# Kernel tuning notes

Measured on AMD Instinct MI355X. Metric: run time of the kernel, lower is better.

The kernel has to match this reference:

```python
import jax, jax.numpy as jnp
import numpy as np

B, T, P, H, D = 8, 16, 14, 16, 64
L = P * P            # 196 patches (CLS excluded)
DM = H * D           # 1024 = d_model
NS = 16              # n_synos
T2 = T * T           # 256 = n_frames**2


def _conv2d(x, w, b):
    # x: [N,C,H,W], w: [O,I,kh,kw], stride 1, SAME padding (ksize//2 for odd k)
    y = jax.lax.conv_general_dilated(x, w, (1, 1), 'SAME',
                                     dimension_numbers=('NCHW', 'OIHW', 'NCHW'))
    return y + b[None, :, None, None]


def _layernorm(x, g, b):
    m = x.mean(-1, keepdims=True)
    v = x.var(-1, keepdims=True)
    return (x - m) / jnp.sqrt(v + 1e-5) * g + b


def setup_inputs() -> dict:
    key = jax.random.key(0)
    ks = jax.random.split(key, 12)
    q = jax.random.normal(ks[0], (B, T, L + 1, H, D), jnp.float32)
    k = jax.random.normal(ks[1], (B, T, L + 1, H, D), jnp.float32)
    v = jax.random.normal(ks[2], (B, T, L + 1, H, D), jnp.float32)
    syno_emb = jax.random.normal(ks[3], (NS, DM), jnp.float32) * 0.02
    t_conv_w = jax.random.normal(ks[4], (1, 2 * H, 3, 3), jnp.float32) * 0.001
    t_conv_b = jnp.zeros((1,), jnp.float32)
    ln_g = jnp.ones((T2,), jnp.float32)
    ln_b = jnp.zeros((T2,), jnp.float32)
    w1 = jax.random.normal(ks[5], (T2, T2), jnp.float32) * 0.02
    b1 = jnp.zeros((T2,), jnp.float32)
    w2 = jax.random.normal(ks[6], (T2, T2), jnp.float32) * 0.02
    b2 = jnp.zeros((T2,), jnp.float32)
    p_conv_w = jax.random.normal(ks[7], (1, T2, 3, 3), jnp.float32) * 0.001
    p_conv_b = jnp.zeros((1,), jnp.float32)
    return dict(q=q, k=k, v=v, syno_emb=syno_emb,
                t_conv_w=t_conv_w, t_conv_b=t_conv_b,
                ln_g=ln_g, ln_b=ln_b, w1=w1, b1=b1, w2=w2, b2=b2,
                p_conv_w=p_conv_w, p_conv_b=p_conv_b)


def reference(q, k, v, syno_emb, t_conv_w, t_conv_b, ln_g, ln_b,
              w1, b1, w2, b2, p_conv_w, p_conv_b):
    # ---------------- temporal detection ----------------
    def head_aff(a):  # a: [B,T,L,H,D] -> [B*L, H, T, T]
        a = a.transpose(0, 2, 1, 3, 4)  # [B,L,T,H,D]
        scale = 1.0 / (a.shape[-1] ** 0.5)
        aff = jnp.einsum('nlqhc,nlkhc->nlqkh', a * scale, a)  # [B,L,T,T,H]
        aff = jax.nn.softmax(aff, axis=-2)  # softmax over key frames
        return aff.reshape(B * L, T, T, H).transpose(0, 3, 1, 2)

    affs = jnp.concatenate([head_aff(q[:, :, 1:]), head_aff(k[:, :, 1:])],
                           axis=1)                      # [B*L, 2H, T, T]
    aff = _conv2d(affs, t_conv_w, t_conv_b)             # [B*L, 1, T, T]
    aff = aff.reshape(B, P, P, T2)                      # [B, P, P, T^2]
    h = _layernorm(aff, ln_g, ln_b)
    h = h @ w1.T + b1
    h = jax.nn.gelu(h, approximate=False)               # torch nn.GELU default
    h = h @ w2.T + b2
    aff = aff + h
    aff = aff.transpose(0, 3, 1, 2)                     # [B, T^2, P, P]
    aff = _conv2d(aff, p_conv_w, p_conv_b)              # [B, 1, P, P]
    y_t = aff.reshape(B, -1)                            # [B, P*P]

    # ---------------- spatial detection ----------------
    kf = k[:, :, 1:].reshape(B, T, L, DM)
    vf = v[:, :, 1:].reshape(B, T, L, DM)
    s_scale = 1.0 / (DM ** 0.5)
    s_aff = jnp.einsum('qw,ntkw->ntqk', syno_emb * s_scale, kf)  # [B,T,NS,L]
    s_aff = jax.nn.softmax(s_aff, axis=-1)
    s_mix = jnp.einsum('ntql,ntlw->ntqw', s_aff, vf)    # [B,T,NS,DM]
    y_s = s_mix.reshape(B, T * NS, DM).mean(axis=1)     # [B, DM]

    return (y_t, y_s)
```

## Files before the change

kernel.cpp:

```cpp
#include <hip/hip_runtime.h>
#include <hip/hip_bf16.h>
#include <math.h>

#define BB 8
#define TT 16
#define PP 14
#define LL 196
#define HH 16
#define DD 64
#define DM 1024
#define NS 16
#define T2 256
#define LP1 197

using bf16x8 = __attribute__((ext_vector_type(8))) short;
using f32x4  = __attribute__((ext_vector_type(4))) float;

__device__ __forceinline__ float dot4(float4 a, float4 b) {
    return a.x*b.x + a.y*b.y + a.z*b.z + a.w*b.w;
}

__device__ __forceinline__ uint32_t pkbf(float lo, float hi) {
    uint32_t a = __builtin_bit_cast(uint32_t, lo);
    uint32_t b = __builtin_bit_cast(uint32_t, hi);
    a += 0x7FFFu + ((a >> 16) & 1u);
    b += 0x7FFFu + ((b >> 16) & 1u);
    return (a >> 16) | (b & 0xFFFF0000u);
}

__device__ __forceinline__ void split2(float x, float y, uint32_t* h, uint32_t* lo) {
    const uint32_t hh = pkbf(x, y);
    const float hx = __builtin_bit_cast(float, hh << 16);
    const float hy = __builtin_bit_cast(float, hh & 0xFFFF0000u);
    *h = hh;
    *lo = pkbf(x - hx, y - hy);
}

__device__ __forceinline__ void pksplit(float4 p, float4 q, bf16x8& hi, bf16x8& lo) {
    uint32_t uh[4], ul[4];
    split2(p.x, p.y, &uh[0], &ul[0]);
    split2(p.z, p.w, &uh[1], &ul[1]);
    split2(q.x, q.y, &uh[2], &ul[2]);
    split2(q.z, q.w, &uh[3], &ul[3]);
    struct U4 { uint32_t v[4]; } th, tl;
    th.v[0] = uh[0]; th.v[1] = uh[1]; th.v[2] = uh[2]; th.v[3] = uh[3];
    tl.v[0] = ul[0]; tl.v[1] = ul[1]; tl.v[2] = ul[2]; tl.v[3] = ul[3];
    hi = __builtin_bit_cast(bf16x8, th);
    lo = __builtin_bit_cast(bf16x8, tl);
}

__global__ __launch_bounds__(256) void kprep(
        const float* __restrict__ syno,
        uint32_t* __restrict__ synoHi, uint32_t* __restrict__ synoLo) {
    const int i = blockIdx.x * 256 + threadIdx.x;
    const float x = syno[2 * i], y = syno[2 * i + 1];
    uint32_t h, lo;
    split2(x, y, &h, &lo);
    synoHi[i] = h;
    synoLo[i] = lo;
}

__global__ __launch_bounds__(256) void k1_temporal(
        const float* __restrict__ qin, const float* __restrict__ kin,
        const float* __restrict__ tw,  const float* __restrict__ tbv,
        const uint32_t* __restrict__ synoHi, const uint32_t* __restrict__ synoLo,
        float* __restrict__ affRaw, float* __restrict__ SLout) {
    __shared__ __align__(16) float lds_c[256 * 36];
    __shared__ __align__(16) float lds_wf[9 * 32];
    __shared__ __align__(16) float sl_part[4][16][16];

    const int bid = blockIdx.x, b = bid / LL, l = bid % LL;
    const int tid = threadIdx.x, wid = tid >> 6, lane = tid & 63;
    const int mrow = lane & 15;
    const int g = lane >> 4;

    for (int i = tid; i < 288; i += 256) {
        const int kk = i >> 5, ch = i & 31;
        lds_wf[kk * 32 + ch] = tw[ch * 9 + kk];
    }

    const size_t rowbase = ((size_t)(b*TT + mrow)*LP1 + 1 + l)*DM + g*8;
    f32x4 acc_sl = {0.f, 0.f, 0.f, 0.f};

    #pragma unroll
    for (int j = 0; j < 4; ++j) {
        #pragma unroll
        for (int hf = 0; hf < 2; ++hf) {
            const int ch = 2*wid + 8*j + hf;
            const float* sp2 = (ch < 16) ? qin : kin;
            const float* base = sp2 + rowbase + (size_t)(ch & 15)*DD;
            const float4 a0 = *reinterpret_cast<const float4*>(base);
            const float4 a1 = *reinterpret_cast<const float4*>(base + 4);
            const float4 a2 = *reinterpret_cast<const float4*>(base + 32);
            const float4 a3 = *reinterpret_cast<const float4*>(base + 36);
            bf16x8 h1, l1, h2, l2;
            pksplit(a0, a1, h1, l1);
            pksplit(a2, a3, h2, l2);
            f32x4 acc = {0.f, 0.f, 0.f, 0.f};
            acc = __builtin_amdgcn_mfma_f32_16x16x32_bf16(h1, h1, acc, 0, 0, 0);
            acc = __builtin_amdgcn_mfma_f32_16x16x32_bf16(h1, l1, acc, 0, 0, 0);
            acc = __builtin_amdgcn_mfma_f32_16x16x32_bf16(l1, h1, acc, 0, 0, 0);
            acc = __builtin_amdgcn_mfma_f32_16x16x32_bf16(h2, h2, acc, 0, 0, 0);
            acc = __builtin_amdgcn_mfma_f32_16x16x32_bf16(h2, l2, acc, 0, 0, 0);
            acc = __builtin_amdgcn_mfma_f32_16x16x32_bf16(l2, h2, acc, 0, 0, 0);
            if (ch >= 16) {
                const int off = (lane & 15) * 512 + (ch - 16) * 32 + g * 4;
                const bf16x8 sh1 = *reinterpret_cast<const bf16x8*>(synoHi + off);
                const bf16x8 sl1 = *reinterpret_cast<const bf16x8*>(synoLo + off);
                const bf16x8 sh2 = *reinterpret_cast<const bf16x8*>(synoHi + off + 16);
                const bf16x8 sl2 = *reinterpret_cast<const bf16x8*>(synoLo + off + 16);
                acc_sl = __builtin_amdgcn_mfma_f32_16x16x32_bf16(h1, sh1, acc_sl, 0, 0, 0);
                acc_sl = __builtin_amdgcn_mfma_f32_16x16x32_bf16(h1, sl1, acc_sl, 0, 0, 0);
                acc_sl = __builtin_amdgcn_mfma_f32_16x16x32_bf16(l1, sh1, acc_sl, 0, 0, 0);
                acc_sl = __builtin_amdgcn_mfma_f32_16x16x32_bf16(h2, sh2, acc_sl, 0, 0, 0);
                acc_sl = __builtin_amdgcn_mfma_f32_16x16x32_bf16(h2, sl2, acc_sl, 0, 0, 0);
                acc_sl = __builtin_amdgcn_mfma_f32_16x16x32_bf16(l2, sh2, acc_sl, 0, 0, 0);
            }
            const float x0 = acc[0]*0.125f, x1 = acc[1]*0.125f;
            const float x2 = acc[2]*0.125f, x3 = acc[3]*0.125f;
            float m0 = x0, m1 = x1, m2 = x2, m3 = x3;
            #pragma unroll
            for (int msk = 1; msk < 16; msk <<= 1) {
                m0 = fmaxf(m0, __shfl_xor(m0, msk, 64));
                m1 = fmaxf(m1, __shfl_xor(m1, msk, 64));
                m2 = fmaxf(m2, __shfl_xor(m2, msk, 64));
                m3 = fmaxf(m3, __shfl_xor(m3, msk, 64));
            }
            const float e0 = __expf(x0 - m0), e1 = __expf(x1 - m1);
            const float e2 = __expf(x2 - m2), e3 = __expf(x3 - m3);
            float s0 = e0, s1 = e1, s2 = e2, s3 = e3;
            #pragma unroll
            for (int msk = 1; msk < 16; msk <<= 1) {
                s0 += __shfl_xor(s0, msk, 64);
                s1 += __shfl_xor(s1, msk, 64);
                s2 += __shfl_xor(s2, msk, 64);
                s3 += __shfl_xor(s3, msk, 64);
            }
            const int colb = lane & 15;
            lds_c[((g*4 + 0)*16 + colb)*36 + ch] = e0 / s0;
            lds_c[((g*4 + 1)*16 + colb)*36 + ch] = e1 / s1;
            lds_c[((g*4 + 2)*16 + colb)*36 + ch] = e2 / s2;
            lds_c[((g*4 + 3)*16 + colb)*36 + ch] = e3 / s3;
        }
    }
    #pragma unroll
    for (int r = 0; r < 4; ++r)
        sl_part[wid][g * 4 + r][lane & 15] = acc_sl[r];
    __syncthreads();

    const int oq = tid >> 4, ok = tid & 15;
    float accv = tbv[0];
    #pragma unroll
    for (int ky = 0; ky < 3; ++ky) {
        const int iq = oq + ky - 1;
        if (iq < 0 || iq > 15) continue;
        #pragma unroll
        for (int kx = 0; kx < 3; ++kx) {
            const int ik = ok + kx - 1;
            if (ik < 0 || ik > 15) continue;
            const float4* dp = reinterpret_cast<const float4*>(lds_c + (iq*16 + ik)*36);
            const float4* wp = reinterpret_cast<const float4*>(lds_wf + (ky*3 + kx)*32);
            #pragma unroll
            for (int c4 = 0; c4 < 8; ++c4) accv += dot4(dp[c4], wp[c4]);
        }
    }
    affRaw[(size_t)bid * T2 + tid] = accv;

    {
        const int t = tid >> 4, qq = tid & 15;
        const float s = sl_part[0][t][qq] + sl_part[1][t][qq] +
                        sl_part[2][t][qq] + sl_part[3][t][qq];
        SLout[((size_t)(b * TT + t) * NS + qq) * LL + l] = s * 0.03125f;
    }
}

__global__ __launch_bounds__(256) void k2_mlp(
        const float* __restrict__ affRaw,
        const float* __restrict__ lng, const float* __restrict__ lnb,
        const float* __restrict__ w1, const float* __restrict__ b1,
        const float* __restrict__ w2, const float* __restrict__ b2,
        float* __restrict__ affRes) {
    __shared__ __align__(16) float lx[4 * 256];
    __shared__ __align__(16) float lln[4 * 256];
    __shared__ __align__(16) float lg[4 * 256];
    const int tid = threadIdx.x;
    const int wave = tid >> 6, lane = tid & 63;
    const int i0 = blockIdx.x * 4;
    {
        const float* xr = affRaw + (size_t)(i0 + wave) * 256;
        float4 x = reinterpret_cast<const float4*>(xr)[lane];
        float sm = x.x + x.y + x.z + x.w;
        float ss = x.x * x.x + x.y * x.y + x.z * x.z + x.w * x.w;
        #pragma unroll
        for (int m = 1; m < 64; m <<= 1) {
            sm += __shfl_xor(sm, m, 64);
            ss += __shfl_xor(ss, m, 64);
        }
        const float mean = sm * (1.f / 256.f);
        const float var = ss * (1.f / 256.f) - mean * mean;
        const float inv = rsqrtf(var + 1e-5f);
        const float4 g4 = reinterpret_cast<const float4*>(lng)[lane];
        const float4 bb = reinterpret_cast<const float4*>(lnb)[lane];
        float4 ln;
        ln.x = (x.x - mean) * inv * g4.x + bb.x;
        ln.y = (x.y - mean) * inv * g4.y + bb.y;
        ln.z = (x.z - mean) * inv * g4.z + bb.z;
        ln.w = (x.w - mean) * inv * g4.w + bb.w;
        reinterpret_cast<float4*>(lx + wave * 256)[lane] = x;
        reinterpret_cast<float4*>(lln + wave * 256)[lane] = ln;
    }
    __syncthreads();
    const int j = tid;
    float a0 = 0.f, a1 = 0.f, a2 = 0.f, a3 = 0.f;
    {
        const float4* wr = reinterpret_cast<const float4*>(w1 + (size_t)j * 256);
        const float4* l0 = reinterpret_cast<const float4*>(lln);
        const float4* l1 = reinterpret_cast<const float4*>(lln + 256);
        const float4* l2 = reinterpret_cast<const float4*>(lln + 512);
        const float4* l3 = reinterpret_cast<const float4*>(lln + 768);
        #pragma unroll 8
        for (int m4 = 0; m4 < 64; ++m4) {
            const float4 w = wr[m4];
            a0 += dot4(w, l0[m4]); a1 += dot4(w, l1[m4]);
            a2 += dot4(w, l2[m4]); a3 += dot4(w, l3[m4]);
        }
    }
    const float bj = b1[j];
    const float kInvSqrt2 = 0.70710678118654752f;
    float h0 = a0 + bj, h1 = a1 + bj, h2 = a2 + bj, h3 = a3 + bj;
    lg[0 * 256 + j] = 0.5f * h0 * (1.f + erff(h0 * kInvSqrt2));
    lg[1 * 256 + j] = 0.5f * h1 * (1.f + erff(h1 * kInvSqrt2));
    lg[2 * 256 + j] = 0.5f * h2 * (1.f + erff(h2 * kInvSqrt2));
    lg[3 * 256 + j] = 0.5f * h3 * (1.f + erff(h3 * kInvSqrt2));
    __syncthreads();
    a0 = a1 = a2 = a3 = 0.f;
    {
        const float4* wr = reinterpret_cast<const float4*>(w2 + (size_t)j * 256);
        const float4* l0 = reinterpret_cast<const float4*>(lg);
        const float4* l1 = reinterpret_cast<const float4*>(lg + 256);
        const float4* l2 = reinterpret_cast<const float4*>(lg + 512);
        const float4* l3 = reinterpret_cast<const float4*>(lg + 768);
        #pragma unroll 8
        for (int m4 = 0; m4 < 64; ++m4) {
            const float4 w = wr[m4];
            a0 += dot4(w, l0[m4]); a1 += dot4(w, l1[m4]);
            a2 += dot4(w, l2[m4]); a3 += dot4(w, l3[m4]);
        }
    }
    const float b2j = b2[j];
    affRes[(size_t)(i0 + 0) * 256 + j] = lx[0 * 256 + j] + a0 + b2j;
    affRes[(size_t)(i0 + 1) * 256 + j] = lx[1 * 256 + j] + a1 + b2j;
    affRes[(size_t)(i0 + 2) * 256 + j] = lx[2 * 256 + j] + a2 + b2j;
    affRes[(size_t)(i0 + 3) * 256 + j] = lx[3 * 256 + j] + a3 + b2j;
}

__global__ __launch_bounds__(256) void k3a_pconv(
        const float* __restrict__ affRes, const float* __restrict__ pw,
        float* __restrict__ part) {
    __shared__ __align__(16) float lpw[576];
    const int b = blockIdx.x >> 2, cc = blockIdx.x & 3;
    const int tid = threadIdx.x;
    for (int idx = tid; idx < 576; idx += 256) {
        const int kk = idx / 64, c = idx & 63;
        lpw[kk * 64 + c] = pw[(size_t)(cc * 64 + c) * 9 + kk];
    }
    __syncthreads();
    if (tid < 196) {
        const int p1 = tid / 14, p2 = tid % 14;
        float s = 0.f;
        #pragma unroll
        for (int ky = 0; ky < 3; ++ky) {
            const int ip1 = p1 + ky - 1;
            if (ip1 < 0 || ip1 > 13) continue;
            #pragma unroll
            for (int kx = 0; kx < 3; ++kx) {
                const int ip2 = p2 + kx - 1;
                if (ip2 < 0 || ip2 > 13) continue;
                const float4* ar = reinterpret_cast<const float4*>(
                    affRes + (size_t)(b * LL + ip1 * 14 + ip2) * 256 + cc * 64);
                const float4* wr = reinterpret_cast<const float4*>(lpw + (ky * 3 + kx) * 64);
                #pragma unroll
                for (int c4 = 0; c4 < 16; ++c4) s += dot4(ar[c4], wr[c4]);
            }
        }
        part[(cc * 8 + b) * 196 + tid] = s;
    }
}

__global__ void k3b_yt(const float* __restrict__ part,
                       const float* __restrict__ pcb, float* __restrict__ out) {
    const int b = blockIdx.x, tid = threadIdx.x;
    if (tid < 196) {
        float s = pcb[0];
        #pragma unroll
        for (int cc = 0; cc < 4; ++cc) s += part[(cc * 8 + b) * 196 + tid];
        out[b * 196 + tid] = s;
    }
}

__global__ __launch_bounds__(256) void k4b_softmax(
        const float* __restrict__ SL, float* __restrict__ WSUM) {
    __shared__ float lp[16 * 200];
    const int t = blockIdx.x, b = blockIdx.y;
    const int tid = threadIdx.x;
    const int qq = tid >> 4, j = tid & 15;
    const float* row = SL + (size_t)((b * TT + t) * NS + qq) * LL;
    float v[13];
    float m = -1e30f;
    #pragma unroll
    for (int i = 0; i < 13; ++i) {
        const int l = j + i * 16;
        v[i] = (l < LL) ? row[l] : -1e30f;
        m = fmaxf(m, v[i]);
    }
    #pragma unroll
    for (int msk = 1; msk < 16; msk <<= 1) m = fmaxf(m, __shfl_xor(m, msk, 64));
    float s = 0.f;
    #pragma unroll
    for (int i = 0; i < 13; ++i) {
        const int l = j + i * 16;
        v[i] = (l < LL) ? __expf(v[i] - m) : 0.f;
        s += v[i];
    }
    #pragma unroll
    for (int msk = 1; msk < 16; msk <<= 1) s += __shfl_xor(s, msk, 64);
    const float inv = 1.f / s;
    #pragma unroll
    for (int i = 0; i < 13; ++i) {
        const int l = j + i * 16;
        if (l < LL) lp[qq * 200 + l] = v[i] * inv;
    }
    __syncthreads();
    if (tid < LL) {
        float w = 0.f;
        #pragma unroll
        for (int qi = 0; qi < 16; ++qi) w += lp[qi * 200 + tid];
        WSUM[(size_t)(b * TT + t) * LL + tid] = w;
    }
}

__global__ __launch_bounds__(256) void k4c_vsum(
        const float* __restrict__ vin, const float* __restrict__ WSUM,
        float* __restrict__ PS) {
    __shared__ float lw[98];
    const int t = blockIdx.x, b = blockIdx.y, z = blockIdx.z;
    const int tid = threadIdx.x;
    const int bt = b * TT + t;
    if (tid < 98) lw[tid] = WSUM[(size_t)bt * LL + z * 98 + tid];
    __syncthreads();
    float4 acc = make_float4(0.f, 0.f, 0.f, 0.f);
    const float* vb = vin + ((size_t)bt * LP1 + 1 + z * 98) * DM + tid * 4;
    #pragma unroll 4
    for (int l = 0; l < 98; ++l) {
        const float4 v = *reinterpret_cast<const float4*>(vb + (size_t)l * DM);
        const float w = lw[l];
        acc.x += w * v.x; acc.y += w * v.y; acc.z += w * v.z; acc.w += w * v.w;
    }
    *reinterpret_cast<float4*>(PS + ((size_t)bt * 2 + z) * DM + tid * 4) = acc;
}

__global__ void k4d_ys(const float* __restrict__ PS, float* __restrict__ out) {
    const int i = blockIdx.x * 256 + threadIdx.x;
    const int b = i >> 10, w = i & 1023;
    float s = 0.f;
    #pragma unroll
    for (int tz = 0; tz < 32; ++tz) s += PS[((size_t)b * 32 + tz) * DM + w];
    out[1568 + i] = s * (1.f / 256.f);
}

extern "C" void kernel_launch(void* const* d_in, const int* in_sizes, int n_in,
                              void* d_out, int out_size, void* d_ws, size_t ws_size,
                              hipStream_t stream) {
    const float* q    = (const float*)d_in[0];
    const float* k    = (const float*)d_in[1];
    const float* v    = (const float*)d_in[2];
    const float* syno = (const float*)d_in[3];
    const float* tw   = (const float*)d_in[4];
    const float* tbv  = (const float*)d_in[5];
    const float* lng  = (const float*)d_in[6];
    const float* lnb  = (const float*)d_in[7];
    const float* w1   = (const float*)d_in[8];
    const float* b1   = (const float*)d_in[9];
    const float* w2   = (const float*)d_in[10];
    const float* b2   = (const float*)d_in[11];
    const float* pw   = (const float*)d_in[12];
    const float* pcb  = (const float*)d_in[13];
    float* out = (float*)d_out;

    float* ws = (float*)d_ws;
    float* affRaw = ws;
    float* affRes = ws + 401408;
    float* SL     = ws + 802816;
    float* WSUM   = ws + 1204224;
    float* part   = ws + 1229312;
    uint32_t* synoHi = (uint32_t*)(ws + 1235584);
    uint32_t* synoLo = (uint32_t*)(ws + 1243776);
    float* PS     = ws;

    hipLaunchKernelGGL(kprep, dim3(32), dim3(256), 0, stream, syno, synoHi, synoLo);
    hipLaunchKernelGGL(k1_temporal, dim3(BB * LL), dim3(256), 0, stream,
                       q, k, tw, tbv, synoHi, synoLo, affRaw, SL);
    hipLaunchKernelGGL(k2_mlp, dim3(392), dim3(256), 0, stream,
                       affRaw, lng, lnb, w1, b1, w2, b2, affRes);
    hipLaunchKernelGGL(k3a_pconv, dim3(32), dim3(256), 0, stream,
                       affRes, pw, part);
    hipLaunchKernelGGL(k3b_yt, dim3(8), dim3(256), 0, stream, part, pcb, out);
    hipLaunchKernelGGL(k4b_softmax, dim3(16, 8), dim3(256), 0, stream, SL, WSUM);
    hipLaunchKernelGGL(k4c_vsum, dim3(16, 8, 2), dim3(256), 0, stream, v, WSUM, PS);
    hipLaunchKernelGGL(k4d_ys, dim3(32), dim3(256), 0, stream, PS, out);
}
```

Measured before the change: 157.8 us.

## Split temporal conv into two channel passes with smaller channel-major LDS buffer

The 32-channel affinity buffer in LDS becomes a 16-channel, channel-major buffer with padded stride, and the block processes q channels and k channels in two passes, running the 3x3 conv partially after each pass. Conv weights are now read directly from global memory (uniform, cacheable) instead of being staged in LDS. This cuts LDS use per block to raise occupancy and changes the bank access pattern. In exchange it adds an extra barrier per pass, loses the vectorized float4 conv reads, and issues scalar weight loads.

Result: faster. 149.3 us (-5.4%).

```diff
diff --git a/kernel.cpp b/kernel.cpp
--- a/kernel.cpp
+++ b/kernel.cpp
@@ -65,104 +65,106 @@
         const float* __restrict__ tw,  const float* __restrict__ tbv,
         const uint32_t* __restrict__ synoHi, const uint32_t* __restrict__ synoLo,
         float* __restrict__ affRaw, float* __restrict__ SLout) {
-    __shared__ __align__(16) float lds_c[256 * 36];
-    __shared__ __align__(16) float lds_wf[9 * 32];
+    __shared__ __align__(16) float lds_c[16 * 260];
     __shared__ __align__(16) float sl_part[4][16][16];
 
     const int bid = blockIdx.x, b = bid / LL, l = bid % LL;
     const int tid = threadIdx.x, wid = tid >> 6, lane = tid & 63;
     const int mrow = lane & 15;
     const int g = lane >> 4;
-
-    for (int i = tid; i < 288; i += 256) {
-        const int kk = i >> 5, ch = i & 31;
-        lds_wf[kk * 32 + ch] = tw[ch * 9 + kk];
-    }
+    const int colb = lane & 15;
+    const int oq = tid >> 4, ok = tid & 15;
 
     const size_t rowbase = ((size_t)(b*TT + mrow)*LP1 + 1 + l)*DM + g*8;
     f32x4 acc_sl = {0.f, 0.f, 0.f, 0.f};
-
-    #pragma unroll
-    for (int j = 0; j < 4; ++j) {
-        #pragma unroll
-        for (int hf = 0; hf < 2; ++hf) {
-            const int ch = 2*wid + 8*j + hf;
-            const float* sp2 = (ch < 16) ? qin : kin;
-            const float* base = sp2 + rowbase + (size_t)(ch & 15)*DD;
-            const float4 a0 = *reinterpret_cast<const float4*>(base);
-            const float4 a1 = *reinterpret_cast<const float4*>(base + 4);
-            const float4 a2 = *reinterpret_cast<const float4*>(base + 32);
-            const float4 a3 = *reinterpret_cast<const float4*>(base + 36);
-            bf16x8 h1, l1, h2, l2;
-            pksplit(a0, a1, h1, l1);
-            pksplit(a2, a3, h2, l2);
-            f32x4 acc = {0.f, 0.f, 0.f, 0.f};
-            acc = __builtin_amdgcn_mfma_f32_16x16x32_bf16(h1, h1, acc, 0, 0, 0);
-            acc = __builtin_amdgcn_mfma_f32_16x16x32_bf16(h1, l1, acc, 0, 0, 0);
-            acc = __builtin_amdgcn_mfma_f32_16x16x32_bf16(l1, h1, acc, 0, 0, 0);
-            acc = __builtin_amdgcn_mfma_f32_16x16x32_bf16(h2, h2, acc, 0, 0, 0);
-            acc = __builtin_amdgcn_mfma_f32_16x16x32_bf16(h2, l2, acc, 0, 0, 0);
-            acc = __builtin_amdgcn_mfma_f32_16x16x32_bf16(l2, h2, acc, 0, 0, 0);
-            if (ch >= 16) {
-                const int off = (lane & 15) * 512 + (ch - 16) * 32 + g * 4;
-                const bf16x8 sh1 = *reinterpret_cast<const bf16x8*>(synoHi + off);
-                const bf16x8 sl1 = *reinterpret_cast<const bf16x8*>(synoLo + off);
-                const bf16x8 sh2 = *reinterpret_cast<const bf16x8*>(synoHi + off + 16);
-                const bf16x8 sl2 = *reinterpret_cast<const bf16x8*>(synoLo + off + 16);
-                acc_sl = __builtin_amdgcn_mfma_f32_16x16x32_bf16(h1, sh1, acc_sl, 0, 0, 0);
-                acc_sl = __builtin_amdgcn_mfma_f32_16x16x32_bf16(h1, sl1, acc_sl, 0, 0, 0);
-                acc_sl = __builtin_amdgcn_mfma_f32_16x16x32_bf16(l1, sh1, acc_sl, 0, 0, 0);
-                acc_sl = __builtin_amdgcn_mfma_f32_16x16x32_bf16(h2, sh2, acc_sl, 0, 0, 0);
-                acc_sl = __builtin_amdgcn_mfma_f32_16x16x32_bf16(h2, sl2, acc_sl, 0, 0, 0);
-                acc_sl = __builtin_amdgcn_mfma_f32_16x16x32_bf16(l2, sh2, acc_sl, 0, 0, 0);
+    float accv = tbv[0];
+
+    #pragma unroll
+    for (int pass = 0; pass < 2; ++pass) {
+        #pragma unroll
+        for (int jj = 0; jj < 2; ++jj) {
+            const int j = pass * 2 + jj;
+            #pragma unroll
+            for (int hf = 0; hf < 2; ++hf) {
+                const int ch = 2*wid + 8*j + hf;
+                const float* sp2 = (pass == 0) ? qin : kin;
+                const float* base = sp2 + rowbase + (size_t)(ch & 15)*DD;
+                const float4 a0 = *reinterpret_cast<const float4*>(base);
+                const float4 a1 = *reinterpret_cast<const float4*>(base + 4);
+                const float4 a2 = *reinterpret_cast<const float4*>(base + 32);
+                const float4 a3 = *reinterpret_cast<const float4*>(base + 36);
+                bf16x8 h1, l1, h2, l2;
+                pksplit(a0, a1, h1, l1);
+                pksplit(a2, a3, h2, l2);
+                f32x4 acc = {0.f, 0.f, 0.f, 0.f};
+                acc = __builtin_amdgcn_mfma_f32_16x16x32_bf16(h1, h1, acc, 0, 0, 0);
+                acc = __builtin_amdgcn_mfma_f32_16x16x32_bf16(h1, l1, acc, 0, 0, 0);
+                acc = __builtin_amdgcn_mfma_f32_16x16x32_bf16(l1, h1, acc, 0, 0, 0);
+                acc = __builtin_amdgcn_mfma_f32_16x16x32_bf16(h2, h2, acc, 0, 0, 0);
+                acc = __builtin_amdgcn_mfma_f32_16x16x32_bf16(h2, l2, acc, 0, 0, 0);
+                acc = __builtin_amdgcn_mfma_f32_16x16x32_bf16(l2, h2, acc, 0, 0, 0);
+                if (pass == 1) {
+                    const int off = colb * 512 + (ch - 16) * 32 + g * 4;
+                    const bf16x8 sh1 = *reinterpret_cast<const bf16x8*>(synoHi + off);
+                    const bf16x8 sl1 = *reinterpret_cast<const bf16x8*>(synoLo + off);
+                    const bf16x8 sh2 = *reinterpret_cast<const bf16x8*>(synoHi + off + 16);
+                    const bf16x8 sl2 = *reinterpret_cast<const bf16x8*>(synoLo + off + 16);
+                    acc_sl = __builtin_amdgcn_mfma_f32_16x16x32_bf16(h1, sh1, acc_sl, 0, 0, 0);
+                    acc_sl = __builtin_amdgcn_mfma_f32_16x16x32_bf16(h1, sl1, acc_sl, 0, 0, 0);
+                    acc_sl = __builtin_amdgcn_mfma_f32_16x16x32_bf16(l1, sh1, acc_sl, 0, 0, 0);
+                    acc_sl = __builtin_amdgcn_mfma_f32_16x16x32_bf16(h2, sh2, acc_sl, 0, 0, 0);
+                    acc_sl = __builtin_amdgcn_mfma_f32_16x16x32_bf16(h2, sl2, acc_sl, 0, 0, 0);
+                    acc_sl = __builtin_amdgcn_mfma_f32_16x16x32_bf16(l2, sh2, acc_sl, 0, 0, 0);
+                }
+                const float x0 = acc[0]*0.125f, x1 = acc[1]*0.125f;
+                const float x2 = acc[2]*0.125f, x3 = acc[3]*0.125f;
+                float m0 = x0, m1 = x1, m2 = x2, m3 = x3;
+                #pragma unroll
+                for (int msk = 1; msk < 16; msk <<= 1) {
+                    m0 = fmaxf(m0, __shfl_xor(m0, msk, 64));
+                    m1 = fmaxf(m1, __shfl_xor(m1, msk, 64));
+                    m2 = fmaxf(m2, __shfl_xor(m2, msk, 64));
+                    m3 = fmaxf(m3, __shfl_xor(m3, msk, 64));
+                }
+                const float e0 = __expf(x0 - m0), e1 = __expf(x1 - m1);
+                const float e2 = __expf(x2 - m2), e3 = __expf(x3 - m3);
+                float s0 = e0, s1 = e1, s2 = e2, s3 = e3;
+                #pragma unroll
+                for (int msk = 1; msk < 16; msk <<= 1) {
+                    s0 += __shfl_xor(s0, msk, 64);
+                    s1 += __shfl_xor(s1, msk, 64);
+                    s2 += __shfl_xor(s2, msk, 64);
+                    s3 += __shfl_xor(s3, msk, 64);
+                }
+                const int slot = 2*wid + 8*jj + hf;
+                float* cp = lds_c + slot * 260;
+                cp[(g*4 + 0)*16 + colb] = e0 / s0;
+                cp[(g*4 + 1)*16 + colb] = e1 / s1;
+                cp[(g*4 + 2)*16 + colb] = e2 / s2;
+                cp[(g*4 + 3)*16 + colb] = e3 / s3;
             }
-            const float x0 = acc[0]*0.125f, x1 = acc[1]*0.125f;
-            const float x2 = acc[2]*0.125f, x3 = acc[3]*0.125f;
-            float m0 = x0, m1 = x1, m2 = x2, m3 = x3;
+        }
+        if (pass == 1) {
             #pragma unroll
-            for (int msk = 1; msk < 16; msk <<= 1) {
-                m0 = fmaxf(m0, __shfl_xor(m0, msk, 64));
-                m1 = fmaxf(m1, __shfl_xor(m1, msk, 64));
-                m2 = fmaxf(m2, __shfl_xor(m2, msk, 64));
-                m3 = fmaxf(m3, __shfl_xor(m3, msk, 64));
+            for (int r = 0; r < 4; ++r)
+                sl_part[wid][g * 4 + r][colb] = acc_sl[r];
+        }
+        __syncthreads();
+        #pragma unroll
+        for (int ky = 0; ky < 3; ++ky) {
+            const int iq = oq + ky - 1;
+            if (iq < 0 || iq > 15) continue;
+            #pragma unroll
+            for (int kx = 0; kx < 3; ++kx) {
+                const int ik = ok + kx - 1;
+                if (ik < 0 || ik > 15) continue;
+                const int pix = iq * 16 + ik;
+                #pragma unroll
+                for (int s = 0; s < 16; ++s)
+                    accv += lds_c[s * 260 + pix] * tw[(pass*16 + s)*9 + ky*3 + kx];
             }
-            const float e0 = __expf(x0 - m0), e1 = __expf(x1 - m1);
-            const float e2 = __expf(x2 - m2), e3 = __expf(x3 - m3);
-            float s0 = e0, s1 = e1, s2 = e2, s3 = e3;
-            #pragma unroll
-            for (int msk = 1; msk < 16; msk <<= 1) {
-                s0 += __shfl_xor(s0, msk, 64);
-                s1 += __shfl_xor(s1, msk, 64);
-                s2 += __shfl_xor(s2, msk, 64);
-                s3 += __shfl_xor(s3, msk, 64);
-            }
-            const int colb = lane & 15;
-            lds_c[((g*4 + 0)*16 + colb)*36 + ch] = e0 / s0;
-            lds_c[((g*4 + 1)*16 + colb)*36 + ch] = e1 / s1;
-            lds_c[((g*4 + 2)*16 + colb)*36 + ch] = e2 / s2;
-            lds_c[((g*4 + 3)*16 + colb)*36 + ch] = e3 / s3;
-        }
-    }
-    #pragma unroll
-    for (int r = 0; r < 4; ++r)
-        sl_part[wid][g * 4 + r][lane & 15] = acc_sl[r];
-    __syncthreads();
-
-    const int oq = tid >> 4, ok = tid & 15;
-    float accv = tbv[0];
-    #pragma unroll
-    for (int ky = 0; ky < 3; ++ky) {
-        const int iq = oq + ky - 1;
-        if (iq < 0 || iq > 15) continue;
-        #pragma unroll
-        for (int kx = 0; kx < 3; ++kx) {
-            const int ik = ok + kx - 1;
-            if (ik < 0 || ik > 15) continue;
-            const float4* dp = reinterpret_cast<const float4*>(lds_c + (iq*16 + ik)*36);
-            const float4* wp = reinterpret_cast<const float4*>(lds_wf + (ky*3 + kx)*32);
-            #pragma unroll
-            for (int c4 = 0; c4 < 8; ++c4) accv += dot4(dp[c4], wp[c4]);
-        }
+        }
+        if (pass == 0) __syncthreads();
     }
     affRaw[(size_t)bid * T2 + tid] = accv;
 
```
